# Kernel optimization log

Hardware: AMD Instinct MI355X
Metric: run time of the kernel (lower is better)

The kernel has to match this reference:

```python
import jax, jax.numpy as jnp
import numpy as np

B, N, C = 8, 4096, 512
NH = 8
HD = C // NH
EPS = 1e-12  # torch F.normalize default eps


def setup_inputs() -> dict:
    key = jax.random.key(0)
    ks = jax.random.split(key, 6)
    x = jax.random.normal(ks[0], (B, N, C), dtype=jnp.float32)
    x_out = jax.random.normal(ks[1], (B, N, C), dtype=jnp.float32)
    # params: torch Linear weight [out,in]; store as [in,out] for x @ W
    W_qkv = jax.random.normal(ks[2], (C, 3 * C), dtype=jnp.float32) * (1.0 / np.sqrt(C))
    temperature = jnp.ones((NH, 1, 1), dtype=jnp.float32)
    W_proj = jax.random.normal(ks[3], (C, C), dtype=jnp.float32) * (1.0 / np.sqrt(C))
    b_proj = jax.random.normal(ks[4], (C,), dtype=jnp.float32) * 0.01
    return {"x": x, "x_out": x_out, "W_qkv": W_qkv, "temperature": temperature,
            "W_proj": W_proj, "b_proj": b_proj, "H": 64, "W": 64}


def _l2norm(t):
    # F.normalize(t, dim=-1): t / max(||t||_2, eps)
    n = jnp.sqrt(jnp.sum(t * t, axis=-1, keepdims=True))
    return t / jnp.maximum(n, EPS)


def reference(x, x_out, W_qkv, temperature, W_proj, b_proj, H, W):
    b, n, c = x.shape
    nh = temperature.shape[0]
    hd = c // nh
    qkv = (x @ W_qkv).reshape(b, n, 3, nh, hd).transpose(2, 0, 3, 1, 4)  # [3,B,nh,N,hd]
    q, k, v = qkv[0], qkv[1], qkv[2]
    # transpose to channel-attention layout [B,nh,hd,N]
    q = jnp.swapaxes(q, -2, -1)
    k = jnp.swapaxes(k, -2, -1)
    v = jnp.swapaxes(v, -2, -1)
    q = _l2norm(q)
    k = _l2norm(k)
    # cross-covariance attention over channels: [B,nh,hd,hd]
    attn = jnp.einsum('bhcn,bhdn->bhcd', q, k) * temperature
    attn = jax.nn.softmax(attn, axis=-1)
    out = jnp.einsum('bhcd,bhdn->bhcn', attn, v)  # [B,nh,hd,N]
    out = out.transpose(0, 3, 1, 2).reshape(b, n, c)
    return out @ W_proj + b_proj
```

## Files before the change

kernel.cpp:

```cpp
#include <hip/hip_runtime.h>
#include <hip/hip_bf16.h>

typedef __attribute__((ext_vector_type(8))) short short8;
typedef __attribute__((ext_vector_type(4))) float f32x4;

#define BQ 8
#define SEQ 4096
#define CH 512
#define NHD 8
#define HD 64
#define K3C 1536
#define MTOK 32768
#define NSPL 8

__device__ __forceinline__ float bfu2f(unsigned int u) {
  u <<= 16;
  float f;
  __builtin_memcpy(&f, &u, 4);
  return f;
}
__device__ __forceinline__ unsigned short f2bfu(float x) {
  __hip_bfloat16 h = __float2bfloat16(x);
  unsigned short u;
  __builtin_memcpy(&u, &h, 2);
  return u;
}

__device__ __forceinline__ void gload_lds16(const void* g, void* l) {
  __builtin_amdgcn_global_load_lds(
      (const __attribute__((address_space(1))) unsigned int*)g,
      (__attribute__((address_space(3))) unsigned int*)l, 16, 0, 0);
}

__global__ __launch_bounds__(256) void cast_f32_bf16(const float* __restrict__ in,
                                                     unsigned short* __restrict__ out, int n4) {
  int stride = gridDim.x * blockDim.x;
  for (int i = blockIdx.x * blockDim.x + threadIdx.x; i < n4; i += stride) {
    float4 v = reinterpret_cast<const float4*>(in)[i];
    ushort4 o;
    o.x = f2bfu(v.x); o.y = f2bfu(v.y); o.z = f2bfu(v.z); o.w = f2bfu(v.w);
    reinterpret_cast<ushort4*>(out)[i] = o;
  }
}

__global__ __launch_bounds__(256) void transpose_cast(const float* __restrict__ in,
                                                      unsigned short* __restrict__ out,
                                                      int R, int Cc) {
  __shared__ float tile[32][33];
  const int tx = threadIdx.x, ty = threadIdx.y;
  const int c0 = blockIdx.x * 32, r0 = blockIdx.y * 32;
  #pragma unroll
  for (int dy = 0; dy < 32; dy += 8)
    tile[ty + dy][tx] = in[(size_t)(r0 + ty + dy) * Cc + (c0 + tx)];
  __syncthreads();
  #pragma unroll
  for (int dy = 0; dy < 32; dy += 8)
    out[(size_t)(c0 + ty + dy) * R + (r0 + tx)] = f2bfu(tile[tx][ty + dy]);
}

template <int MODE>
__global__ __launch_bounds__(512, 4) void gemm256(const unsigned short* __restrict__ A,
                                                  const unsigned short* __restrict__ Bt,
                                                  void* __restrict__ out0,
                                                  void* __restrict__ out1,
                                                  const float* __restrict__ bias,
                                                  int M, int Nn, int Kk, int nbx) {
  __shared__ __align__(16) char lds[73728];
  const int nwg = gridDim.x;
  int wg = blockIdx.x;
  wg = (wg & 7) * (nwg >> 3) + (wg >> 3);
  const int bx = wg % nbx, by = wg / nbx;
  const int m0 = by * 256, n0 = bx * 128;

  const int tid = threadIdx.x, wave = tid >> 6, lane = tid & 63;
  const int wr = wave >> 1, wc = wave & 1;
  const int l15 = lane & 15, lg = lane >> 4;
  const int T = Kk >> 5;

  f32x4 acc[4][4] = {};
  short8 af[4], bf[4];

  const int prowA = tid >> 3, sA = tid & 7;
  const int slinA = sA ^ (prowA & 7);
  const int mA = ((slinA >> 2) << 7) + prowA, kA = (slinA & 3) << 3;
  const int prow2 = prowA + 64;
  const int slin2 = sA ^ (prow2 & 7);
  const int m2 = ((slin2 >> 2) << 7) + prow2, k2 = (slin2 & 3) << 3;
  const int prowB = tid >> 3, sB = tid & 7;
  const int slinB = sB ^ (prowB & 7);
  const int nB = ((slinB >> 2) << 6) + prowB, kB = (slinB & 3) << 3;
  const int woff = wave * 1024;

  auto stageAB = [&](int kt, char* buf) {
    gload_lds16(A + (size_t)(m0 + mA) * Kk + kt + kA, buf + woff);
    gload_lds16(A + (size_t)(m0 + m2) * Kk + kt + k2, buf + 8192 + woff);
    gload_lds16(Bt + (size_t)(n0 + nB) * Kk + kt + kB, buf + 16384 + woff);
  };

  auto dsA = [&](const char* bufc) {
    #pragma unroll
    for (int fr = 0; fr < 4; ++fr) {
      const int m = wr * 64 + fr * 16 + l15;
      const int prow = m & 127;
      const int s = ((m >> 7) * 4 + lg) ^ (l15 & 7);
      af[fr] = *reinterpret_cast<const short8*>(bufc + prow * 128 + (s << 4));
    }
  };
  auto dsB = [&](const char* bufc) {
    #pragma unroll
    for (int fc = 0; fc < 4; ++fc) {
      const int prow = fc * 16 + l15;
      const int s = (wc * 4 + lg) ^ (l15 & 7);
      bf[fc] = *reinterpret_cast<const short8*>(bufc + 16384 + prow * 128 + (s << 4));
    }
  };

  stageAB(0, lds);
  stageAB(32, lds + 24576);
  asm volatile("s_waitcnt vmcnt(3)" ::: "memory");
  __builtin_amdgcn_s_barrier();

  char* p0 = lds;
  char* p1 = lds + 24576;
  char* p2 = lds + 49152;

  for (int t = 0; t < T; ++t) {
    dsA(p0);
    dsB(p0);
    const bool st2 = (t + 2 < T);
    if (st2) stageAB((t + 2) << 5, p2);
    __builtin_amdgcn_s_setprio(1);
    #pragma unroll
    for (int fr = 0; fr < 4; ++fr)
      #pragma unroll
      for (int fc = 0; fc < 4; ++fc)
        acc[fr][fc] = __builtin_amdgcn_mfma_f32_16x16x32_bf16(
            af[fr], bf[fc], acc[fr][fc], 0, 0, 0);
    __builtin_amdgcn_s_setprio(0);
    if (t + 1 < T) {
      if (st2) asm volatile("s_waitcnt vmcnt(3)" ::: "memory");
      else     asm volatile("s_waitcnt vmcnt(0)" ::: "memory");
      __builtin_amdgcn_s_barrier();
    }
    char* tmp = p0; p0 = p1; p1 = p2; p2 = tmp;
  }

  if (MODE == 1) {
    #pragma unroll
    for (int fr = 0; fr < 4; ++fr)
      #pragma unroll
      for (int fc = 0; fc < 4; ++fc) {
        const int row0 = m0 + wr * 64 + fr * 16 + lg * 4;
        const int col = n0 + wc * 64 + fc * 16 + l15;
        #pragma unroll
        for (int v = 0; v < 4; ++v)
          reinterpret_cast<float*>(out0)[(size_t)(row0 + v) * Nn + col] =
              acc[fr][fc][v] + bias[col];
      }
  } else if (n0 < 1024) {
    #pragma unroll
    for (int p = 0; p < 2; ++p) {
      __builtin_amdgcn_s_barrier();
      if (wc == p) {
        #pragma unroll
        for (int fr = 0; fr < 4; ++fr)
          #pragma unroll
          for (int fc = 0; fc < 4; ++fc) {
            const int tok = wr * 64 + fr * 16 + lg * 4;
            const int cl = fc * 16 + l15;
            ushort4 o;
            o.x = f2bfu(acc[fr][fc][0]);
            o.y = f2bfu(acc[fr][fc][1]);
            o.z = f2bfu(acc[fr][fc][2]);
            o.w = f2bfu(acc[fr][fc][3]);
            const int byte = cl * 512 + ((tok * 2) ^ ((cl & 7) << 4));
            *reinterpret_cast<ushort4*>(lds + byte) = o;
          }
      }
      __builtin_amdgcn_s_barrier();
      #pragma unroll
      for (int it = 0; it < 4; ++it) {
        const int cl = it * 16 + (tid >> 5);
        const int ns = (tid & 31) * 8;
        const int byte = cl * 512 + ((ns * 2) ^ ((cl & 7) << 4));
        short8 val = *reinterpret_cast<const short8*>(lds + byte);
        const int gcol = n0 + p * 64 + cl;
        const int sel = gcol >> 9, rem = gcol & 511;
        const int bh = (m0 >> 12) * 8 + (rem >> 6), cc = rem & 63;
        *reinterpret_cast<short8*>(&reinterpret_cast<unsigned short*>(out0)[
            ((size_t)sel * 4096 + bh * 64 + cc) * 4096 + (m0 & 4095) + ns]) = val;
      }
    }
  } else {
    #pragma unroll
    for (int fr = 0; fr < 4; ++fr)
      #pragma unroll
      for (int fc = 0; fc < 4; ++fc) {
        const int row0 = m0 + wr * 64 + fr * 16 + lg * 4;
        const int col = n0 + wc * 64 + fc * 16 + l15;
        const int rem = col & 511, hh = rem >> 6, cc = rem & 63;
        const int bb = row0 >> 12, nseq = row0 & 4095;
        const int bh = bb * 8 + hh;
        #pragma unroll
        for (int v = 0; v < 4; ++v)
          reinterpret_cast<unsigned short*>(out1)[
              ((size_t)bh * 4096 + nseq + v) * 64 + cc] =
              f2bfu(acc[fr][fc][v]);
      }
  }
}

__global__ __launch_bounds__(256) void attn_qk(const unsigned short* __restrict__ qkT,
                                               float* __restrict__ rawp,
                                               float* __restrict__ normp) {
  const int bh = blockIdx.x, s = blockIdx.y;
  const int tid = threadIdx.x, w = tid >> 6, lane = tid & 63;
  const int l15 = lane & 15, lg = lane >> 4;
  const int nbase = s * 512 + w * 128;
  const unsigned short* qrow = qkT + (size_t)(bh * 64) * 4096;
  const unsigned short* krow = qkT + (size_t)(4096 + bh * 64) * 4096;

  __shared__ float red[4][64][64];
  __shared__ float nrm[4][2][64];

  f32x4 acc[4][4] = {};
  float sq[4] = {0.f, 0.f, 0.f, 0.f}, sk[4] = {0.f, 0.f, 0.f, 0.f};

  #pragma unroll
  for (int kc = 0; kc < 2; ++kc) {
    short8 aq[4][2], bk[4][2];
    #pragma unroll
    for (int fr = 0; fr < 4; ++fr)
      #pragma unroll
      for (int ks = 0; ks < 2; ++ks) {
        const size_t off = (size_t)(fr * 16 + l15) * 4096 + nbase + (kc * 2 + ks) * 32 + lg * 8;
        aq[fr][ks] = *reinterpret_cast<const short8*>(&qrow[off]);
        bk[fr][ks] = *reinterpret_cast<const short8*>(&krow[off]);
      }
    #pragma unroll
    for (int ks = 0; ks < 2; ++ks)
      #pragma unroll
      for (int fr = 0; fr < 4; ++fr)
        #pragma unroll
        for (int fc = 0; fc < 4; ++fc)
          acc[fr][fc] = __builtin_amdgcn_mfma_f32_16x16x32_bf16(
              aq[fr][ks], bk[fc][ks], acc[fr][fc], 0, 0, 0);
    #pragma unroll
    for (int fr = 0; fr < 4; ++fr)
      #pragma unroll
      for (int ks = 0; ks < 2; ++ks)
        #pragma unroll
        for (int j = 0; j < 8; ++j) {
          const float fq = bfu2f((unsigned short)aq[fr][ks][j]);
          const float fk = bfu2f((unsigned short)bk[fr][ks][j]);
          sq[fr] = fmaf(fq, fq, sq[fr]);
          sk[fr] = fmaf(fk, fk, sk[fr]);
        }
  }

  #pragma unroll
  for (int fr = 0; fr < 4; ++fr) {
    sq[fr] += __shfl_xor(sq[fr], 16); sq[fr] += __shfl_xor(sq[fr], 32);
    sk[fr] += __shfl_xor(sk[fr], 16); sk[fr] += __shfl_xor(sk[fr], 32);
  }
  if (lane < 16) {
    #pragma unroll
    for (int fr = 0; fr < 4; ++fr) {
      nrm[w][0][fr * 16 + lane] = sq[fr];
      nrm[w][1][fr * 16 + lane] = sk[fr];
    }
  }
  #pragma unroll
  for (int fr = 0; fr < 4; ++fr)
    #pragma unroll
    for (int fc = 0; fc < 4; ++fc)
      #pragma unroll
      for (int v = 0; v < 4; ++v)
        red[w][fr * 16 + lg * 4 + v][fc * 16 + l15] = acc[fr][fc][v];
  __syncthreads();

  const float* rf = &red[0][0][0];
  float* rp = rawp + ((size_t)s * 64 + bh) * 4096;
  for (int i = tid; i < 4096; i += 256)
    rp[i] = rf[i] + rf[4096 + i] + rf[8192 + i] + rf[12288 + i];
  const float* nf = &nrm[0][0][0];
  if (tid < 128) {
    float* np = normp + ((size_t)s * 64 + bh) * 128;
    np[tid] = nf[tid] + nf[128 + tid] + nf[256 + tid] + nf[384 + tid];
  }
}

__global__ __launch_bounds__(64) void attn_finalize(const float* __restrict__ rawp,
                                                    const float* __restrict__ normp,
                                                    const float* __restrict__ temperature,
                                                    unsigned short* __restrict__ attnP) {
  const int bh = blockIdx.x, c8 = blockIdx.y, h = bh & 7;
  const int d = threadIdx.x;
  float nq = 0.f, nk = 0.f;
  for (int s = 0; s < NSPL; ++s) {
    nq += normp[((size_t)s * 64 + bh) * 128 + d];
    nk += normp[((size_t)s * 64 + bh) * 128 + 64 + d];
  }
  nq = fmaxf(sqrtf(nq), 1e-12f);
  nk = fmaxf(sqrtf(nk), 1e-12f);
  const float t = temperature[h];
  for (int i = 0; i < 8; ++i) {
    const int c = c8 * 8 + i;
    float r = 0.f;
    for (int s = 0; s < NSPL; ++s)
      r += rawp[((size_t)s * 64 + bh) * 4096 + c * 64 + d];
    const float nqc = __shfl(nq, c);
    float v = r * t / (nqc * nk);
    float m = v;
    #pragma unroll
    for (int off = 32; off > 0; off >>= 1) m = fmaxf(m, __shfl_xor(m, off));
    float e = __expf(v - m);
    float ssum = e;
    #pragma unroll
    for (int off = 32; off > 0; off >>= 1) ssum += __shfl_xor(ssum, off);
    attnP[(size_t)bh * 4096 + c * 64 + d] = f2bfu(e / ssum);
  }
}

__global__ __launch_bounds__(256) void pv_mfma(const unsigned short* __restrict__ attnP,
                                               const unsigned short* __restrict__ vb,
                                               unsigned short* __restrict__ y) {
  const int nc = blockIdx.x, bh = blockIdx.y;
  const int b = bh >> 3, h = bh & 7;
  const int tid = threadIdx.x, w = tid >> 6, lane = tid & 63;
  const int l15 = lane & 15, lg = lane >> 4;
  const int n0 = nc * 256 + w * 64;

  short8 ap[4][2], bv[4][2];
  #pragma unroll
  for (int fr = 0; fr < 4; ++fr)
    #pragma unroll
    for (int ks = 0; ks < 2; ++ks)
      ap[fr][ks] = *reinterpret_cast<const short8*>(
          &attnP[(size_t)bh * 4096 + (fr * 16 + l15) * 64 + ks * 32 + lg * 8]);
  #pragma unroll
  for (int fc = 0; fc < 4; ++fc)
    #pragma unroll
    for (int ks = 0; ks < 2; ++ks)
      bv[fc][ks] = *reinterpret_cast<const short8*>(
          &vb[((size_t)bh * 4096 + n0 + fc * 16 + l15) * 64 + ks * 32 + lg * 8]);

  f32x4 acc[4][4] = {};
  #pragma unroll
  for (int ks = 0; ks < 2; ++ks)
    #pragma unroll
    for (int fr = 0; fr < 4; ++fr)
      #pragma unroll
      for (int fc = 0; fc < 4; ++fc)
        acc[fr][fc] = __builtin_amdgcn_mfma_f32_16x16x32_bf16(
            ap[fr][ks], bv[fc][ks], acc[fr][fc], 0, 0, 0);

  #pragma unroll
  for (int fr = 0; fr < 4; ++fr)
    #pragma unroll
    for (int fc = 0; fc < 4; ++fc) {
      const int n = n0 + fc * 16 + l15;
      const int c0 = fr * 16 + lg * 4;
      ushort4 o;
      o.x = f2bfu(acc[fr][fc][0]); o.y = f2bfu(acc[fr][fc][1]);
      o.z = f2bfu(acc[fr][fc][2]); o.w = f2bfu(acc[fr][fc][3]);
      *reinterpret_cast<ushort4*>(
          &y[((size_t)b * 4096 + n) * 512 + h * 64 + c0]) = o;
    }
}

extern "C" void kernel_launch(void* const* d_in, const int* in_sizes, int n_in,
                              void* d_out, int out_size, void* d_ws, size_t ws_size,
                              hipStream_t stream) {
  const float* x = (const float*)d_in[0];
  const float* Wqkv = (const float*)d_in[2];
  const float* temp = (const float*)d_in[3];
  const float* Wproj = (const float*)d_in[4];
  const float* bproj = (const float*)d_in[5];
  float* out = (float*)d_out;

  char* w = (char*)d_ws;
  unsigned short* xb = (unsigned short*)w;    w += (size_t)MTOK * CH * 2;
  unsigned short* wqT = (unsigned short*)w;   w += (size_t)K3C * CH * 2;
  unsigned short* wpT = (unsigned short*)w;   w += (size_t)CH * CH * 2;
  unsigned short* qkT = (unsigned short*)w;   w += (size_t)2 * 64 * 64 * 4096 * 2;
  unsigned short* vb = (unsigned short*)w;    w += (size_t)64 * 4096 * 64 * 2;
  unsigned short* yb = (unsigned short*)w;    w += (size_t)MTOK * CH * 2;
  float* rawp = (float*)w;                    w += (size_t)NSPL * 64 * 4096 * 4;
  float* normp = (float*)w;                   w += (size_t)NSPL * 64 * 128 * 4;
  unsigned short* attnP = (unsigned short*)w; w += (size_t)64 * 4096 * 2;

  cast_f32_bf16<<<2048, 256, 0, stream>>>(x, xb, MTOK * CH / 4);
  transpose_cast<<<dim3(K3C / 32, CH / 32), dim3(32, 8), 0, stream>>>(Wqkv, wqT, CH, K3C);
  transpose_cast<<<dim3(CH / 32, CH / 32), dim3(32, 8), 0, stream>>>(Wproj, wpT, CH, CH);
  gemm256<0><<<1536, 512, 0, stream>>>(xb, wqT, qkT, vb, nullptr, MTOK, K3C, CH, 12);
  attn_qk<<<dim3(64, 8), 256, 0, stream>>>(qkT, rawp, normp);
  attn_finalize<<<dim3(64, 8), 64, 0, stream>>>(rawp, normp, temp, attnP);
  pv_mfma<<<dim3(16, 64), 256, 0, stream>>>(attnP, vb, yb);
  gemm256<1><<<512, 512, 0, stream>>>(yb, wpT, out, nullptr, bproj, MTOK, CH, CH, 4);
}
```

Measured before the change: 158.1 us.

## Fold attention matrix into projection weights, skip PV kernel and y buffer

Uses associativity: out = V^T·(attn^T·W_proj), so a per-batch modified weight W_mod = attn^T-block times W_proj is computed in a small kernel and the final GEMM reads V directly with per-batch weights. This removes the PV matmul kernel and the write and read of the intermediate y tensor, along with the separate W_proj transpose. In exchange a per-batch 512x512 bf16 weight matrix is built and the final GEMM has to index V in its per-head layout, which changes its load addressing and may reduce weight reuse in L2.

```diff
diff --git a/kernel.cpp b/kernel.cpp
--- a/kernel.cpp
+++ b/kernel.cpp
@@ -91,10 +91,22 @@
   const int nB = ((slinB >> 2) << 6) + prowB, kB = (slinB & 3) << 3;
   const int woff = wave * 1024;
 
+  const int bidx = m0 >> 12;
+  const unsigned short* Bt2 = Bt + (size_t)bidx * 262144;
+  const int nrow1 = (m0 & 4095) + mA, nrow2 = (m0 & 4095) + m2;
+
   auto stageAB = [&](int kt, char* buf) {
-    gload_lds16(A + (size_t)(m0 + mA) * Kk + kt + kA, buf + woff);
-    gload_lds16(A + (size_t)(m0 + m2) * Kk + kt + k2, buf + 8192 + woff);
-    gload_lds16(Bt + (size_t)(n0 + nB) * Kk + kt + kB, buf + 16384 + woff);
+    if (MODE == 2) {
+      const unsigned short* Abase =
+          A + (size_t)(bidx * 8 + (kt >> 6)) * 4096 * 64 + (kt & 32);
+      gload_lds16(Abase + (size_t)nrow1 * 64 + kA, buf + woff);
+      gload_lds16(Abase + (size_t)nrow2 * 64 + k2, buf + 8192 + woff);
+      gload_lds16(Bt2 + (size_t)(n0 + nB) * Kk + kt + kB, buf + 16384 + woff);
+    } else {
+      gload_lds16(A + (size_t)(m0 + mA) * Kk + kt + kA, buf + woff);
+      gload_lds16(A + (size_t)(m0 + m2) * Kk + kt + k2, buf + 8192 + woff);
+      gload_lds16(Bt + (size_t)(n0 + nB) * Kk + kt + kB, buf + 16384 + woff);
+    }
   };
 
   auto dsA = [&](const char* bufc) {
@@ -145,7 +157,7 @@
     char* tmp = p0; p0 = p1; p1 = p2; p2 = tmp;
   }
 
-  if (MODE == 1) {
+  if (MODE == 2) {
     #pragma unroll
     for (int fr = 0; fr < 4; ++fr)
       #pragma unroll
@@ -293,7 +305,7 @@
 __global__ __launch_bounds__(64) void attn_finalize(const float* __restrict__ rawp,
                                                     const float* __restrict__ normp,
                                                     const float* __restrict__ temperature,
-                                                    unsigned short* __restrict__ attnP) {
+                                                    float* __restrict__ Pmat) {
   const int bh = blockIdx.x, c8 = blockIdx.y, h = bh & 7;
   const int d = threadIdx.x;
   float nq = 0.f, nk = 0.f;
@@ -318,55 +330,32 @@
     float ssum = e;
     #pragma unroll
     for (int off = 32; off > 0; off >>= 1) ssum += __shfl_xor(ssum, off);
-    attnP[(size_t)bh * 4096 + c * 64 + d] = f2bfu(e / ssum);
-  }
-}
-
-__global__ __launch_bounds__(256) void pv_mfma(const unsigned short* __restrict__ attnP,
-                                               const unsigned short* __restrict__ vb,
-                                               unsigned short* __restrict__ y) {
-  const int nc = blockIdx.x, bh = blockIdx.y;
+    Pmat[(size_t)bh * 4096 + c * 64 + d] = e / ssum;
+  }
+}
+
+__global__ __launch_bounds__(256) void wmod_kernel(const float* __restrict__ Pmat,
+                                                   const float* __restrict__ Wproj,
+                                                   unsigned short* __restrict__ WmodT) {
+  const int bh = blockIdx.x, jt = blockIdx.y;
   const int b = bh >> 3, h = bh & 7;
-  const int tid = threadIdx.x, w = tid >> 6, lane = tid & 63;
-  const int l15 = lane & 15, lg = lane >> 4;
-  const int n0 = nc * 256 + w * 64;
-
-  short8 ap[4][2], bv[4][2];
-  #pragma unroll
-  for (int fr = 0; fr < 4; ++fr)
-    #pragma unroll
-    for (int ks = 0; ks < 2; ++ks)
-      ap[fr][ks] = *reinterpret_cast<const short8*>(
-          &attnP[(size_t)bh * 4096 + (fr * 16 + l15) * 64 + ks * 32 + lg * 8]);
-  #pragma unroll
-  for (int fc = 0; fc < 4; ++fc)
-    #pragma unroll
-    for (int ks = 0; ks < 2; ++ks)
-      bv[fc][ks] = *reinterpret_cast<const short8*>(
-          &vb[((size_t)bh * 4096 + n0 + fc * 16 + l15) * 64 + ks * 32 + lg * 8]);
-
-  f32x4 acc[4][4] = {};
-  #pragma unroll
-  for (int ks = 0; ks < 2; ++ks)
-    #pragma unroll
-    for (int fr = 0; fr < 4; ++fr)
-      #pragma unroll
-      for (int fc = 0; fc < 4; ++fc)
-        acc[fr][fc] = __builtin_amdgcn_mfma_f32_16x16x32_bf16(
-            ap[fr][ks], bv[fc][ks], acc[fr][fc], 0, 0, 0);
-
-  #pragma unroll
-  for (int fr = 0; fr < 4; ++fr)
-    #pragma unroll
-    for (int fc = 0; fc < 4; ++fc) {
-      const int n = n0 + fc * 16 + l15;
-      const int c0 = fr * 16 + lg * 4;
-      ushort4 o;
-      o.x = f2bfu(acc[fr][fc][0]); o.y = f2bfu(acc[fr][fc][1]);
-      o.z = f2bfu(acc[fr][fc][2]); o.w = f2bfu(acc[fr][fc][3]);
-      *reinterpret_cast<ushort4*>(
-          &y[((size_t)b * 4096 + n) * 512 + h * 64 + c0]) = o;
-    }
+  const int tid = threadIdx.x;
+  __shared__ float PL[64][64];
+  __shared__ float WT[64][65];
+  for (int i = tid; i < 4096; i += 256) PL[i >> 6][i & 63] = Pmat[(size_t)bh * 4096 + i];
+  for (int i = tid; i < 4096; i += 256) {
+    const int c = i >> 6, j = i & 63;
+    WT[c][j] = Wproj[(size_t)(h * 64 + c) * 512 + jt * 64 + j];
+  }
+  __syncthreads();
+  const int d = tid & 63, jq = tid >> 6;
+  #pragma unroll
+  for (int jl = jq * 16; jl < jq * 16 + 16; ++jl) {
+    float acc = 0.f;
+    #pragma unroll
+    for (int c = 0; c < 64; ++c) acc = fmaf(PL[c][d], WT[c][jl], acc);
+    WmodT[((size_t)b * 512 + jt * 64 + jl) * 512 + h * 64 + d] = f2bfu(acc);
+  }
 }
 
 extern "C" void kernel_launch(void* const* d_in, const int* in_sizes, int n_in,
@@ -382,20 +371,18 @@
   char* w = (char*)d_ws;
   unsigned short* xb = (unsigned short*)w;    w += (size_t)MTOK * CH * 2;
   unsigned short* wqT = (unsigned short*)w;   w += (size_t)K3C * CH * 2;
-  unsigned short* wpT = (unsigned short*)w;   w += (size_t)CH * CH * 2;
   unsigned short* qkT = (unsigned short*)w;   w += (size_t)2 * 64 * 64 * 4096 * 2;
   unsigned short* vb = (unsigned short*)w;    w += (size_t)64 * 4096 * 64 * 2;
-  unsigned short* yb = (unsigned short*)w;    w += (size_t)MTOK * CH * 2;
   float* rawp = (float*)w;                    w += (size_t)NSPL * 64 * 4096 * 4;
   float* normp = (float*)w;                   w += (size_t)NSPL * 64 * 128 * 4;
-  unsigned short* attnP = (unsigned short*)w; w += (size_t)64 * 4096 * 2;
+  float* Pmat = (float*)w;                    w += (size_t)64 * 4096 * 4;
+  unsigned short* WmodT = (unsigned short*)w; w += (size_t)BQ * CH * CH * 2;
 
   cast_f32_bf16<<<2048, 256, 0, stream>>>(x, xb, MTOK * CH / 4);
   transpose_cast<<<dim3(K3C / 32, CH / 32), dim3(32, 8), 0, stream>>>(Wqkv, wqT, CH, K3C);
-  transpose_cast<<<dim3(CH / 32, CH / 32), dim3(32, 8), 0, stream>>>(Wproj, wpT, CH, CH);
   gemm256<0><<<1536, 512, 0, stream>>>(xb, wqT, qkT, vb, nullptr, MTOK, K3C, CH, 12);
   attn_qk<<<dim3(64, 8), 256, 0, stream>>>(qkT, rawp, normp);
-  attn_finalize<<<dim3(64, 8), 64, 0, stream>>>(rawp, normp, temp, attnP);
-  pv_mfma<<<dim3(16, 64), 256, 0, stream>>>(attnP, vb, yb);
-  gemm256<1><<<512, 512, 0, stream>>>(yb, wpT, out, nullptr, bproj, MTOK, CH, CH, 4);
-}
+  attn_finalize<<<dim3(64, 8), 64, 0, stream>>>(rawp, normp, temp, Pmat);
+  wmod_kernel<<<dim3(64, 8), 256, 0, stream>>>(Pmat, Wproj, WmodT);
+  gemm256<2><<<512, 512, 0, stream>>>(vb, WmodT, out, nullptr, bproj, MTOK, CH, CH, 4);
+}
```

Result: no change. 158.6 us (+0.3%).
